# Optimization experiments

Hardware: AMD Instinct MI355X
Metric: run time of the kernel (lower is better)

The kernel has to match this reference:

```python
import jax, jax.numpy as jnp
import numpy as np

T, B, N = 512, 256, 128


def setup_inputs() -> dict:
    key = jax.random.key(0)
    k1, k2, k3, k4, k5, k6 = jax.random.split(key, 6)
    emit = jax.random.normal(k1, (T, B, N), dtype=jnp.float32)
    target = jax.random.randint(k2, (T, B), 0, N, dtype=jnp.int32)
    # monotone mask: each sequence has length in [T//2, T]
    lengths = jax.random.randint(k3, (B,), T // 2, T + 1, dtype=jnp.int32)
    mask = jnp.arange(T, dtype=jnp.int32)[:, None] < lengths[None, :]
    trans = 0.1 * jax.random.normal(k4, (N, N), dtype=jnp.float32)
    strans = 0.1 * jax.random.normal(k5, (N,), dtype=jnp.float32)
    etrans = 0.1 * jax.random.normal(k6, (N,), dtype=jnp.float32)
    return {"emit": emit, "target": target, "mask": mask,
            "trans": trans, "strans": strans, "etrans": etrans}


def _crf_nll(emit, trans, strans, etrans, target, mask):
    t_len, b, n = emit.shape

    # ---- logZ: forward algorithm (sequential scan over time) ----
    def step(alpha, inp):
        emit_i, mask_i = inp  # [B,N], [B]
        # scores[b, j, k] = alpha[b, j] + trans[j, k] + emit_i[b, k]
        scores = jax.nn.logsumexp(
            alpha[:, :, None] + trans[None, :, :] + emit_i[:, None, :], axis=1)
        alpha = jnp.where(mask_i[:, None], scores, alpha)
        return alpha, None

    alpha0 = strans[None, :] + emit[0]  # [B,N]
    alpha, _ = jax.lax.scan(step, alpha0, (emit[1:], mask[1:]))
    logZ = jax.nn.logsumexp(alpha + etrans[None, :], axis=1).sum()

    # ---- gold score ----
    emit_sc = jnp.take_along_axis(emit, target[:, :, None], axis=2)[..., 0]  # [T,B]
    trans_sc = trans[target[:-1], target[1:]]  # [T-1,B]
    scores = emit_sc.at[1:].add(trans_sc)
    score = jnp.where(mask, scores, 0.0).sum()
    ends = mask.sum(axis=0) - 1  # [B]
    score = score + strans[target[0]].sum()
    score = score + etrans[target[ends, jnp.arange(b)]].sum()

    return (logZ - score) / b


def reference(emit, target, mask, trans, strans, etrans):
    return _crf_nll(emit, trans, strans, etrans, target, mask)
```

## Files before the change

### kernel.cpp

```cpp
#include <hip/hip_runtime.h>

#define T_LEN 512
#define B_SZ  256
#define N_ST  128

#if defined(__has_builtin)
# if __has_builtin(__builtin_amdgcn_fdot2_f32_bf16)
#  define HAVE_DOT2 1
# endif
#endif
#ifndef HAVE_DOT2
# define HAVE_DOT2 0
#endif

typedef unsigned int uint32;
typedef __bf16 bf16x2 __attribute__((ext_vector_type(2)));

__device__ __forceinline__ uint32 bf16rn(float f) {
    uint32 u = __builtin_bit_cast(uint32, f);
    u += 0x7fffu + ((u >> 16) & 1u);
    return u >> 16;
}
__device__ __forceinline__ uint32 pack2(float lo, float hi) {
    return bf16rn(lo) | (bf16rn(hi) << 16);
}
__device__ __forceinline__ float dot2b(uint32 a, uint32 b, float c) {
#if HAVE_DOT2
    return __builtin_amdgcn_fdot2_f32_bf16(__builtin_bit_cast(bf16x2, a),
                                           __builtin_bit_cast(bf16x2, b), c, false);
#else
    float alo = __builtin_bit_cast(float, a << 16);
    float ahi = __builtin_bit_cast(float, a & 0xffff0000u);
    float blo = __builtin_bit_cast(float, b << 16);
    float bhi = __builtin_bit_cast(float, b & 0xffff0000u);
    return fmaf(ahi, bhi, fmaf(alo, blo, c));
#endif
}


__global__ __launch_bounds__(64) void lengths_kernel(const unsigned char* __restrict__ mask_raw,
                                                     int* __restrict__ lens) {
    int b = blockIdx.x;
    int l = threadIdx.x;
    unsigned char b1 = mask_raw[1], b2 = mask_raw[2];
    int mode = (b1 != 0) ? 0 : ((b2 != 0) ? 2 : 1);
    int cnt = 0;
    if (mode == 0) {
        #pragma unroll
        for (int k = 0; k < 8; ++k) cnt += (mask_raw[(l * 8 + k) * B_SZ + b] != 0);
    } else if (mode == 1) {
        const int* m = (const int*)mask_raw;
        #pragma unroll
        for (int k = 0; k < 8; ++k) cnt += (m[(l * 8 + k) * B_SZ + b] != 0);
    } else {
        const float* m = (const float*)mask_raw;
        #pragma unroll
        for (int k = 0; k < 8; ++k) cnt += (m[(l * 8 + k) * B_SZ + b] != 0.0f);
    }
    #pragma unroll
    for (int off = 1; off < 64; off <<= 1) cnt += __shfl_xor(cnt, off);
    if (l == 0) lens[b] = cnt;
}

__global__ __launch_bounds__(128, 1) void forward_kernel(
        const float* __restrict__ emit,
        const float* __restrict__ trans,
        const float* __restrict__ strans,
        const float* __restrict__ etrans,
        const int* __restrict__ lens,
        float* __restrict__ logZ_out) {
    const int b   = blockIdx.x;
    const int tid = threadIdx.x;
    const int wid = tid >> 6;
    const int l   = tid & 63;
    const int j0  = l, j1 = l + 64;

    __shared__ alignas(16) unsigned short a16[N_ST];
    __shared__ alignas(16) unsigned short z16[N_ST];
    __shared__ float meetA[N_ST], meetY[N_ST];
    __shared__ float maccSh[2], red2[2];

    const int len = lens[b];
    const int m = (len - 1 < 256) ? (len - 1) : 256;
    const float* eb = emit + (size_t)b * N_ST;
    const size_t TS = (size_t)B_SZ * N_ST;

    if (wid == 0) {
        uint32 EA[64], EB[64];
        #pragma unroll
        for (int p = 0; p < 64; ++p) {
            EA[p] = pack2(__expf(trans[(2 * p) * N_ST + j0]), __expf(trans[(2 * p + 1) * N_ST + j0]));
            EB[p] = pack2(__expf(trans[(2 * p) * N_ST + j1]), __expf(trans[(2 * p + 1) * N_ST + j1]));
        }
        float aA = __expf(strans[j0] + eb[j0]);
        float aB = __expf(strans[j1] + eb[j1]);
        a16[j0] = (unsigned short)bf16rn(aA);
        a16[j1] = (unsigned short)bf16rn(aB);
        float Macc = 0.f, inv = 1.0f;
        float e0 = eb[TS + j0], e1 = eb[TS + j1];
        for (int t = 1; t <= m; ++t) {
            const int tn = (t + 1 <= m) ? t + 1 : m;
            const float en0 = eb[(size_t)tn * TS + j0], en1 = eb[(size_t)tn * TS + j1];
            const float ee0 = __expf(e0), ee1 = __expf(e1);
            float A0 = 0, A1 = 0, A2 = 0, A3 = 0, B0 = 0, B1 = 0, B2 = 0, B3 = 0;
            #pragma unroll
            for (int q = 0; q < 16; ++q) {
                uint4 w;
                __builtin_memcpy(&w, (const char*)a16 + 16 * q, 16);
                A0 = dot2b(w.x, EA[4 * q + 0], A0);  B0 = dot2b(w.x, EB[4 * q + 0], B0);
                A1 = dot2b(w.y, EA[4 * q + 1], A1);  B1 = dot2b(w.y, EB[4 * q + 1], B1);
                A2 = dot2b(w.z, EA[4 * q + 2], A2);  B2 = dot2b(w.z, EB[4 * q + 2], B2);
                A3 = dot2b(w.w, EA[4 * q + 3], A3);  B3 = dot2b(w.w, EB[4 * q + 3], B3);
            }
            const float rA = (A0 + A1) + (A2 + A3);
            const float rB = (B0 + B1) + (B2 + B3);
            Macc -= __logf(inv);
            aA = ee0 * rA * inv;
            aB = ee1 * rB * inv;
            a16[j0] = (unsigned short)bf16rn(aA);
            a16[j1] = (unsigned short)bf16rn(aB);
            inv = __builtin_amdgcn_rcpf(__shfl(rA, 0));
            e0 = en0; e1 = en1;
        }
        meetA[j0] = aA; meetA[j1] = aB;
        if (l == 0) maccSh[0] = Macc;
    } else {
        uint32 RA[64], RB[64];
        #pragma unroll
        for (int p = 0; p < 64; ++p) {
            RA[p] = pack2(__expf(trans[j0 * N_ST + 2 * p]), __expf(trans[j0 * N_ST + 2 * p + 1]));
            RB[p] = pack2(__expf(trans[j1 * N_ST + 2 * p]), __expf(trans[j1 * N_ST + 2 * p + 1]));
        }
        float y0 = __expf(etrans[j0]);
        float y1 = __expf(etrans[j1]);
        float Maccb = 0.f, invb = 1.0f;
        const int t0 = len - 1;
        float e0 = eb[(size_t)t0 * TS + j0], e1 = eb[(size_t)t0 * TS + j1];
        for (int t = t0; t > m; --t) {
            const int tn = (t - 1 > m) ? t - 1 : m + 1;
            const float en0 = eb[(size_t)tn * TS + j0], en1 = eb[(size_t)tn * TS + j1];
            const float ee0 = __expf(e0), ee1 = __expf(e1);
            z16[j0] = (unsigned short)bf16rn(ee0 * y0);
            z16[j1] = (unsigned short)bf16rn(ee1 * y1);
            float R0 = 0, R1 = 0, R2 = 0, R3 = 0, S0 = 0, S1 = 0, S2 = 0, S3 = 0;
            #pragma unroll
            for (int q = 0; q < 16; ++q) {
                uint4 w;
                __builtin_memcpy(&w, (const char*)z16 + 16 * q, 16);
                R0 = dot2b(w.x, RA[4 * q + 0], R0);  S0 = dot2b(w.x, RB[4 * q + 0], S0);
                R1 = dot2b(w.y, RA[4 * q + 1], R1);  S1 = dot2b(w.y, RB[4 * q + 1], S1);
                R2 = dot2b(w.z, RA[4 * q + 2], R2);  S2 = dot2b(w.z, RB[4 * q + 2], S2);
                R3 = dot2b(w.w, RA[4 * q + 3], R3);  S3 = dot2b(w.w, RB[4 * q + 3], S3);
            }
            const float rR = (R0 + R1) + (R2 + R3);
            const float rS = (S0 + S1) + (S2 + S3);
            Maccb -= __logf(invb);
            y0 = rR * invb;
            y1 = rS * invb;
            invb = __builtin_amdgcn_rcpf(__shfl(rR, 0));
            e0 = en0; e1 = en1;
        }
        meetY[j0] = y0; meetY[j1] = y1;
        if (l == 0) maccSh[1] = Maccb;
    }

    __syncthreads();
    float v = meetA[tid] * meetY[tid];
    #pragma unroll
    for (int off = 1; off < 64; off <<= 1) v += __shfl_xor(v, off);
    if (l == 0) red2[wid] = v;
    __syncthreads();
    if (tid == 0) logZ_out[b] = maccSh[0] + maccSh[1] + __logf(red2[0] + red2[1]);
}

__global__ __launch_bounds__(128) void score_kernel(
        const float* __restrict__ emit,
        const int* __restrict__ target,
        const float* __restrict__ trans,
        const float* __restrict__ strans,
        const float* __restrict__ etrans,
        const int* __restrict__ lens,
        float* __restrict__ score_out) {
    const int b   = blockIdx.x;
    const int tid = threadIdx.x;
    const int len = lens[b];
    float local = 0.f;
    for (int t = tid; t < len; t += 128) {
        int tgt = target[t * B_SZ + b];
        float v = emit[(size_t)t * (B_SZ * N_ST) + b * N_ST + tgt];
        if (t > 0) v += trans[target[(t - 1) * B_SZ + b] * N_ST + tgt];
        local += v;
    }
    if (tid == 0) {
        local += strans[target[b]];
        local += etrans[target[(len - 1) * B_SZ + b]];
    }
    #pragma unroll
    for (int off = 1; off < 64; off <<= 1) local += __shfl_xor(local, off);
    __shared__ float partial[2];
    if ((tid & 63) == 0) partial[tid >> 6] = local;
    __syncthreads();
    if (tid == 0) score_out[b] = partial[0] + partial[1];
}

__global__ __launch_bounds__(256) void finalize_kernel(
        const float* __restrict__ logZ,
        const float* __restrict__ score,
        float* __restrict__ out) {
    int tid = threadIdx.x;
    float v = logZ[tid] - score[tid];
    #pragma unroll
    for (int off = 1; off < 64; off <<= 1) v += __shfl_xor(v, off);
    __shared__ float p[4];
    if ((tid & 63) == 0) p[tid >> 6] = v;
    __syncthreads();
    if (tid == 0) out[0] = (p[0] + p[1] + p[2] + p[3]) / 256.0f;
}

extern "C" void kernel_launch(void* const* d_in, const int* in_sizes, int n_in,
                              void* d_out, int out_size, void* d_ws, size_t ws_size,
                              hipStream_t stream) {
    const float*         emit   = (const float*)d_in[0];
    const int*           target = (const int*)d_in[1];
    const unsigned char* mask   = (const unsigned char*)d_in[2];
    const float*         trans  = (const float*)d_in[3];
    const float*         strans = (const float*)d_in[4];
    const float*         etrans = (const float*)d_in[5];

    float* ws     = (float*)d_ws;
    float* logZb  = ws;
    float* scoreb = ws + 256;
    int*   lens   = (int*)(ws + 512);

    lengths_kernel<<<B_SZ, 64, 0, stream>>>(mask, lens);
    forward_kernel<<<B_SZ, 128, 0, stream>>>(emit, trans, strans, etrans, lens, logZb);
    score_kernel<<<B_SZ, 128, 0, stream>>>(emit, target, trans, strans, etrans, lens, scoreb);
    finalize_kernel<<<1, 256, 0, stream>>>(logZb, scoreb, (float*)d_out);
}
```

Before: 133.3 us.

## Pack state as bf16 pairs per lane, prefetch emissions two steps ahead, use readlane

Each lane now owns adjacent states (2l, 2l+1), so the bf16 state vector is written as one packed 32-bit LDS store using a hardware v_cvt_pk_bf16_f32 instruction instead of two 16-bit stores with software rounding. Emission loads are prefetched two timesteps ahead rather than one, to hide more global-memory latency in the serial recurrence. The cross-lane broadcast of the normalizer uses readlane instead of a shuffle. Together these target per-step latency in the sequential forward/backward loops, at the cost of extra registers and a dependency on the inline asm instruction being available.

```diff
diff --git a/kernel.cpp b/kernel.cpp
--- a/kernel.cpp
+++ b/kernel.cpp
@@ -23,6 +23,14 @@
 }
 __device__ __forceinline__ uint32 pack2(float lo, float hi) {
     return bf16rn(lo) | (bf16rn(hi) << 16);
+}
+__device__ __forceinline__ uint32 cvtpk(float lo, float hi) {
+    uint32 r;
+    asm("v_cvt_pk_bf16_f32 %0, %1, %2" : "=v"(r) : "v"(lo), "v"(hi));
+    return r;
+}
+__device__ __forceinline__ float readlane0(float v) {
+    return __builtin_bit_cast(float, (uint32)__builtin_amdgcn_readlane(__builtin_bit_cast(int, v), 0));
 }
 __device__ __forceinline__ float dot2b(uint32 a, uint32 b, float c) {
 #if HAVE_DOT2
@@ -73,10 +81,10 @@
     const int tid = threadIdx.x;
     const int wid = tid >> 6;
     const int l   = tid & 63;
-    const int j0  = l, j1 = l + 64;
-
-    __shared__ alignas(16) unsigned short a16[N_ST];
-    __shared__ alignas(16) unsigned short z16[N_ST];
+    const int c0  = 2 * l, c1 = 2 * l + 1;
+
+    __shared__ alignas(16) uint32 a32[64];
+    __shared__ alignas(16) uint32 z32[64];
     __shared__ float meetA[N_ST], meetY[N_ST];
     __shared__ float maccSh[2], red2[2];
 
@@ -89,24 +97,24 @@
         uint32 EA[64], EB[64];
         #pragma unroll
         for (int p = 0; p < 64; ++p) {
-            EA[p] = pack2(__expf(trans[(2 * p) * N_ST + j0]), __expf(trans[(2 * p + 1) * N_ST + j0]));
-            EB[p] = pack2(__expf(trans[(2 * p) * N_ST + j1]), __expf(trans[(2 * p + 1) * N_ST + j1]));
-        }
-        float aA = __expf(strans[j0] + eb[j0]);
-        float aB = __expf(strans[j1] + eb[j1]);
-        a16[j0] = (unsigned short)bf16rn(aA);
-        a16[j1] = (unsigned short)bf16rn(aB);
+            EA[p] = pack2(__expf(trans[(2 * p) * N_ST + c0]), __expf(trans[(2 * p + 1) * N_ST + c0]));
+            EB[p] = pack2(__expf(trans[(2 * p) * N_ST + c1]), __expf(trans[(2 * p + 1) * N_ST + c1]));
+        }
+        float aA = __expf(strans[c0] + eb[c0]);
+        float aB = __expf(strans[c1] + eb[c1]);
+        a32[l] = pack2(aA, aB);
         float Macc = 0.f, inv = 1.0f;
-        float e0 = eb[TS + j0], e1 = eb[TS + j1];
+        float ec0 = eb[TS + c0],      ec1 = eb[TS + c1];
+        float en0 = eb[2 * TS + c0],  en1 = eb[2 * TS + c1];
         for (int t = 1; t <= m; ++t) {
-            const int tn = (t + 1 <= m) ? t + 1 : m;
-            const float en0 = eb[(size_t)tn * TS + j0], en1 = eb[(size_t)tn * TS + j1];
-            const float ee0 = __expf(e0), ee1 = __expf(e1);
+            const size_t t2 = (size_t)((t + 2 <= m) ? t + 2 : m) * TS;
+            const float e20 = eb[t2 + c0], e21 = eb[t2 + c1];
+            const float ee0 = __expf(ec0), ee1 = __expf(ec1);
             float A0 = 0, A1 = 0, A2 = 0, A3 = 0, B0 = 0, B1 = 0, B2 = 0, B3 = 0;
             #pragma unroll
             for (int q = 0; q < 16; ++q) {
                 uint4 w;
-                __builtin_memcpy(&w, (const char*)a16 + 16 * q, 16);
+                __builtin_memcpy(&w, (const char*)a32 + 16 * q, 16);
                 A0 = dot2b(w.x, EA[4 * q + 0], A0);  B0 = dot2b(w.x, EB[4 * q + 0], B0);
                 A1 = dot2b(w.y, EA[4 * q + 1], A1);  B1 = dot2b(w.y, EB[4 * q + 1], B1);
                 A2 = dot2b(w.z, EA[4 * q + 2], A2);  B2 = dot2b(w.z, EB[4 * q + 2], B2);
@@ -117,36 +125,36 @@
             Macc -= __logf(inv);
             aA = ee0 * rA * inv;
             aB = ee1 * rB * inv;
-            a16[j0] = (unsigned short)bf16rn(aA);
-            a16[j1] = (unsigned short)bf16rn(aB);
-            inv = __builtin_amdgcn_rcpf(__shfl(rA, 0));
-            e0 = en0; e1 = en1;
-        }
-        meetA[j0] = aA; meetA[j1] = aB;
+            a32[l] = cvtpk(aA, aB);
+            inv = __builtin_amdgcn_rcpf(readlane0(rA));
+            ec0 = en0; ec1 = en1; en0 = e20; en1 = e21;
+        }
+        meetA[c0] = aA; meetA[c1] = aB;
         if (l == 0) maccSh[0] = Macc;
     } else {
         uint32 RA[64], RB[64];
         #pragma unroll
         for (int p = 0; p < 64; ++p) {
-            RA[p] = pack2(__expf(trans[j0 * N_ST + 2 * p]), __expf(trans[j0 * N_ST + 2 * p + 1]));
-            RB[p] = pack2(__expf(trans[j1 * N_ST + 2 * p]), __expf(trans[j1 * N_ST + 2 * p + 1]));
-        }
-        float y0 = __expf(etrans[j0]);
-        float y1 = __expf(etrans[j1]);
+            RA[p] = pack2(__expf(trans[c0 * N_ST + 2 * p]), __expf(trans[c0 * N_ST + 2 * p + 1]));
+            RB[p] = pack2(__expf(trans[c1 * N_ST + 2 * p]), __expf(trans[c1 * N_ST + 2 * p + 1]));
+        }
+        float y0 = __expf(etrans[c0]);
+        float y1 = __expf(etrans[c1]);
         float Maccb = 0.f, invb = 1.0f;
         const int t0 = len - 1;
-        float e0 = eb[(size_t)t0 * TS + j0], e1 = eb[(size_t)t0 * TS + j1];
+        float ec0 = eb[(size_t)t0 * TS + c0], ec1 = eb[(size_t)t0 * TS + c1];
+        float en0 = ec0, en1 = ec1;
+        if (t0 - 1 > m) { en0 = eb[(size_t)(t0 - 1) * TS + c0]; en1 = eb[(size_t)(t0 - 1) * TS + c1]; }
         for (int t = t0; t > m; --t) {
-            const int tn = (t - 1 > m) ? t - 1 : m + 1;
-            const float en0 = eb[(size_t)tn * TS + j0], en1 = eb[(size_t)tn * TS + j1];
-            const float ee0 = __expf(e0), ee1 = __expf(e1);
-            z16[j0] = (unsigned short)bf16rn(ee0 * y0);
-            z16[j1] = (unsigned short)bf16rn(ee1 * y1);
+            const int tp = (t - 2 > m) ? t - 2 : m + 1;
+            const float e20 = eb[(size_t)tp * TS + c0], e21 = eb[(size_t)tp * TS + c1];
+            const float ee0 = __expf(ec0), ee1 = __expf(ec1);
+            z32[l] = cvtpk(ee0 * y0, ee1 * y1);
             float R0 = 0, R1 = 0, R2 = 0, R3 = 0, S0 = 0, S1 = 0, S2 = 0, S3 = 0;
             #pragma unroll
             for (int q = 0; q < 16; ++q) {
                 uint4 w;
-                __builtin_memcpy(&w, (const char*)z16 + 16 * q, 16);
+                __builtin_memcpy(&w, (const char*)z32 + 16 * q, 16);
                 R0 = dot2b(w.x, RA[4 * q + 0], R0);  S0 = dot2b(w.x, RB[4 * q + 0], S0);
                 R1 = dot2b(w.y, RA[4 * q + 1], R1);  S1 = dot2b(w.y, RB[4 * q + 1], S1);
                 R2 = dot2b(w.z, RA[4 * q + 2], R2);  S2 = dot2b(w.z, RB[4 * q + 2], S2);
@@ -157,10 +165,10 @@
             Maccb -= __logf(invb);
             y0 = rR * invb;
             y1 = rS * invb;
-            invb = __builtin_amdgcn_rcpf(__shfl(rR, 0));
-            e0 = en0; e1 = en1;
-        }
-        meetY[j0] = y0; meetY[j1] = y1;
+            invb = __builtin_amdgcn_rcpf(readlane0(rR));
+            ec0 = en0; ec1 = en1; en0 = e20; en1 = e21;
+        }
+        meetY[c0] = y0; meetY[c1] = y1;
         if (l == 0) maccSh[1] = Maccb;
     }
 
```

Measured after the change: 125.9 us. 5.6% less time.
